# Kernel tuning notes

Measured on AMD Instinct MI355X. Metric: run time of the kernel, lower is better.

The kernel has to match this reference:

```python
import jax, jax.numpy as jnp
import numpy as np

TEMPERATURE = 0.5
EPS = 1e-12  # matches torch F.normalize default eps


def _l2_normalize(x):
    norm = jnp.sqrt(jnp.sum(x * x, axis=-1, keepdims=True))
    return x / jnp.maximum(norm, EPS)


def setup_inputs() -> dict:
    key = jax.random.key(0)
    k1, k2 = jax.random.split(key)
    B, C, D = 64, 512, 256
    visual_features = jax.random.normal(k1, (B, C, D), dtype=jnp.float32)
    text_embeddings = jax.random.normal(k2, (B, C, D), dtype=jnp.float32)
    return {"visual_features": visual_features, "text_embeddings": text_embeddings}


def reference(visual_features, text_embeddings):
    v = _l2_normalize(visual_features)   # (B, C, D)
    t = _l2_normalize(text_embeddings)   # (B, C, D)
    # positive: diagonal similarity per class
    sim_pos = jnp.einsum('bcd,bcd->bc', v, t)
    positive = jnp.exp(sim_pos / TEMPERATURE)            # (B, C)
    # full BxCxC similarity matrix
    all_sim = jnp.exp(jnp.einsum('bcd,bkd->bck', v, t) / TEMPERATURE)
    negative = jnp.sum(all_sim, axis=-1) - positive      # (B, C)
    loss = -jnp.log(positive / (positive + negative))
    return jnp.mean(loss)
```

## Files before the change

### kernel.cpp

```cpp
#include <hip/hip_runtime.h>
#include <hip/hip_bf16.h>

#define BB 64
#define CC 512
#define DD 256

typedef __attribute__((ext_vector_type(8))) short bf16x8;
typedef __attribute__((ext_vector_type(4))) float f32x4;
typedef unsigned int u32;

#define SWZ(r) (((r) & 7) << 4)

__device__ inline short f2bf(float f) {
    union { __hip_bfloat16 h; short s; } cv;
    cv.h = __float2bfloat16(f);
    return cv.s;
}

__global__ __launch_bounds__(256) void norm_rows(const float* __restrict__ in,
                                                 unsigned short* __restrict__ out) {
    const int row  = blockIdx.x * 4 + (threadIdx.x >> 6);
    const int lane = threadIdx.x & 63;
    const float4 x = reinterpret_cast<const float4*>(in)[(size_t)row * 64 + lane];
    float ss = x.x * x.x + x.y * x.y + x.z * x.z + x.w * x.w;
#pragma unroll
    for (int off = 32; off; off >>= 1) ss += __shfl_xor(ss, off);
    const float r = 1.0f / fmaxf(sqrtf(ss), 1e-12f);
    ushort4 o;
    o.x = (unsigned short)f2bf(x.x * r);
    o.y = (unsigned short)f2bf(x.y * r);
    o.z = (unsigned short)f2bf(x.z * r);
    o.w = (unsigned short)f2bf(x.w * r);
    reinterpret_cast<ushort4*>(out)[(size_t)row * 64 + lane] = o;
}

__global__ __launch_bounds__(256, 2) void gemm_loss(const float* __restrict__ V,
                                                    const unsigned short* __restrict__ Tn,
                                                    float* __restrict__ partials) {
    __shared__ char lds[65536];
    __shared__ float vred[256];
    __shared__ float dred[256];

    const int i0 = blockIdx.x;
    const int b  = (i0 & 7) * 8 + ((i0 >> 3) & 7);
    const int rb = i0 >> 6;

    const int tid  = threadIdx.x;
    const int lane = tid & 63;
    const int wave = tid >> 6;
    const int g    = lane >> 4;
    const int ln   = lane & 15;

    const float* gV = V + (size_t)b * (CC * DD) + (size_t)rb * 64 * DD;
    const char*  gT = reinterpret_cast<const char*>(Tn + (size_t)b * (CC * DD));

#pragma unroll
    for (int r2 = 0; r2 < 8; ++r2) {
        const int L  = r2 * 1024 + (lane << 4);
        const int lr = L >> 9, inrow = L & 511;
        __builtin_amdgcn_global_load_lds(
            (const u32*)(gT + (size_t)(wave * 16 + lr) * 512 + (inrow ^ SWZ(lr))),
            (u32*)(lds + wave * 8192 + r2 * 1024), 16, 0, 0);
    }

    {
        const int rrow  = tid >> 3;
        const int ecolB = (tid & 7) * 64;
        char* bufA = lds + 32768;
#pragma unroll
        for (int p = 0; p < 2; ++p) {
            const float4* src =
                reinterpret_cast<const float4*>(gV + (size_t)(p * 32 + rrow) * DD) + (tid & 7) * 8;
            float4 x[8];
#pragma unroll
            for (int q = 0; q < 8; ++q) x[q] = src[q];
            float ss = 0.f;
#pragma unroll
            for (int q = 0; q < 8; ++q)
                ss += x[q].x * x[q].x + x[q].y * x[q].y + x[q].z * x[q].z + x[q].w * x[q].w;
            ss += __shfl_xor(ss, 1);
            ss += __shfl_xor(ss, 2);
            ss += __shfl_xor(ss, 4);
            const float rinv = 1.0f / fmaxf(sqrtf(ss), 1e-12f);
            const int row = p * 32 + rrow;
            char* dstrow  = bufA + row * 512;
            const int sw  = SWZ(row);
#pragma unroll
            for (int q2 = 0; q2 < 4; ++q2) {
                const float4 v0 = x[2 * q2], v1 = x[2 * q2 + 1];
                bf16x8 o;
                o[0] = f2bf(v0.x * rinv); o[1] = f2bf(v0.y * rinv);
                o[2] = f2bf(v0.z * rinv); o[3] = f2bf(v0.w * rinv);
                o[4] = f2bf(v1.x * rinv); o[5] = f2bf(v1.y * rinv);
                o[6] = f2bf(v1.z * rinv); o[7] = f2bf(v1.w * rinv);
                *reinterpret_cast<bf16x8*>(dstrow + ((ecolB + q2 * 16) ^ sw)) = o;
            }
        }
    }
    __syncthreads();

    bf16x8 a[4][8];
#pragma unroll
    for (int i = 0; i < 4; ++i) {
        const int row  = i * 16 + ln;
        const char* rp = lds + 32768 + row * 512;
        const int sw   = SWZ(row);
#pragma unroll
        for (int kk = 0; kk < 8; ++kk)
            a[i][kk] = *reinterpret_cast<const bf16x8*>(rp + ((kk * 64 + g * 16) ^ sw));
    }
    __syncthreads();

    float rs[4][4];
    float dg[4][4];
#pragma unroll
    for (int i = 0; i < 4; ++i)
#pragma unroll
        for (int r = 0; r < 4; ++r) { rs[i][r] = 0.f; dg[i][r] = 0.f; }

    for (int ct = 0; ct < 8; ++ct) {
        if (ct < 7) {
            const char* gtile = gT + (size_t)(ct + 1) * 64 * 512;
            char* dst = lds + (((ct + 1) & 1) ? 32768 : 0) + wave * 8192;
#pragma unroll
            for (int r2 = 0; r2 < 8; ++r2) {
                const int L  = r2 * 1024 + (lane << 4);
                const int lr = L >> 9, inrow = L & 511;
                __builtin_amdgcn_global_load_lds(
                    (const u32*)(gtile + (size_t)(wave * 16 + lr) * 512 + (inrow ^ SWZ(lr))),
                    (u32*)(dst + r2 * 1024), 16, 0, 0);
            }
            asm volatile("s_waitcnt vmcnt(8)" ::: "memory");
        } else {
            asm volatile("s_waitcnt vmcnt(0)" ::: "memory");
        }

        const char* rp = lds + ((ct & 1) ? 32768 : 0) + wave * 8192 + ln * 512;
        const int sw   = SWZ(ln);
        f32x4 acc[4];
#pragma unroll
        for (int i = 0; i < 4; ++i) acc[i] = (f32x4){0.f, 0.f, 0.f, 0.f};
        __builtin_amdgcn_s_setprio(1);
#pragma unroll
        for (int kk = 0; kk < 8; ++kk) {
            const bf16x8 bb = *reinterpret_cast<const bf16x8*>(rp + ((kk * 64 + g * 16) ^ sw));
#pragma unroll
            for (int i = 0; i < 4; ++i)
                acc[i] = __builtin_amdgcn_mfma_f32_16x16x32_bf16(a[i][kk], bb, acc[i], 0, 0, 0);
        }
        __builtin_amdgcn_s_setprio(0);

        const int gcol = ct * 64 + wave * 16 + ln;
#pragma unroll
        for (int i = 0; i < 4; ++i) {
            const int grow = rb * 64 + i * 16 + g * 4;
#pragma unroll
            for (int r = 0; r < 4; ++r) {
                const float s2 = acc[i][r] * 2.0f;
                rs[i][r] += __expf(s2);
                if (ct == rb && gcol == grow + r) dg[i][r] += s2;
            }
        }
    }

#pragma unroll
    for (int i = 0; i < 4; ++i)
#pragma unroll
        for (int r = 0; r < 4; ++r) {
            float v = rs[i][r];
            float d = dg[i][r];
#pragma unroll
            for (int m = 1; m < 16; m <<= 1) {
                v += __shfl_xor(v, m);
                d += __shfl_xor(d, m);
            }
            if (ln == 0) {
                const int rl = i * 16 + g * 4 + r;
                vred[rl * 4 + wave] = v;
                dred[rl * 4 + wave] = d;
            }
        }
    __syncthreads();

    if (wave == 0) {
        const float vv =
            vred[lane * 4] + vred[lane * 4 + 1] + vred[lane * 4 + 2] + vred[lane * 4 + 3];
        const float dd =
            dred[lane * 4] + dred[lane * 4 + 1] + dred[lane * 4 + 2] + dred[lane * 4 + 3];
        float lsum = logf(vv) - dd;
#pragma unroll
        for (int m = 1; m < 64; m <<= 1) lsum += __shfl_xor(lsum, m);
        if (lane == 0) partials[i0] = lsum;
    }
}

__global__ __launch_bounds__(256) void final_reduce(const float* __restrict__ partials,
                                                    float* __restrict__ out) {
    const int t = threadIdx.x;
    float v = partials[t] + partials[t + 256];
#pragma unroll
    for (int m = 1; m < 64; m <<= 1) v += __shfl_xor(v, m);
    __shared__ float red[4];
    if ((t & 63) == 0) red[t >> 6] = v;
    __syncthreads();
    if (t == 0) out[0] = (red[0] + red[1] + red[2] + red[3]) * (1.0f / 32768.0f);
}

extern "C" void kernel_launch(void* const* d_in, const int* in_sizes, int n_in,
                              void* d_out, int out_size, void* d_ws, size_t ws_size,
                              hipStream_t stream) {
    const float* vis = (const float*)d_in[0];
    const float* txt = (const float*)d_in[1];

    unsigned short* Tn = (unsigned short*)d_ws;
    float* partials    = (float*)((char*)d_ws + (size_t)BB * CC * DD * 2);
    float* out         = (float*)d_out;

    norm_rows<<<8192, 256, 0, stream>>>(txt, Tn);
    gemm_loss<<<512, 256, 0, stream>>>(vis, Tn, partials);
    final_reduce<<<1, 256, 0, stream>>>(partials, out);
}
```

Measured before the change: 40.57 us.

## Halve LDS footprint with 2x2 wave tiling and 32-column double-buffered T tiles

Restructures gemm_loss so each block uses 32KB of LDS instead of 64KB. Waves are arranged 2x2 over the 64-row by 32-column output tile, and T is streamed in 16 tiles of 32 rows through a double buffer that reuses the A staging area. Each wave now holds half as many A fragments and accumulators, and the launch bound is raised to 4 blocks per CU to increase occupancy. The cost is more loop iterations and two explicit barriers per tile, which add synchronisation overhead.

```diff
diff --git a/kernel.cpp b/kernel.cpp
--- a/kernel.cpp
+++ b/kernel.cpp
@@ -34,12 +34,12 @@
     reinterpret_cast<ushort4*>(out)[(size_t)row * 64 + lane] = o;
 }
 
-__global__ __launch_bounds__(256, 2) void gemm_loss(const float* __restrict__ V,
+__global__ __launch_bounds__(256, 4) void gemm_loss(const float* __restrict__ V,
                                                     const unsigned short* __restrict__ Tn,
                                                     float* __restrict__ partials) {
-    __shared__ char lds[65536];
-    __shared__ float vred[256];
-    __shared__ float dred[256];
+    __shared__ char ldsb[32768];
+    __shared__ float vred[128];
+    __shared__ float dred[128];
 
     const int i0 = blockIdx.x;
     const int b  = (i0 & 7) * 8 + ((i0 >> 3) & 7);
@@ -48,25 +48,17 @@
     const int tid  = threadIdx.x;
     const int lane = tid & 63;
     const int wave = tid >> 6;
+    const int wr   = wave >> 1;
+    const int wc   = wave & 1;
     const int g    = lane >> 4;
     const int ln   = lane & 15;
 
     const float* gV = V + (size_t)b * (CC * DD) + (size_t)rb * 64 * DD;
     const char*  gT = reinterpret_cast<const char*>(Tn + (size_t)b * (CC * DD));
-
-#pragma unroll
-    for (int r2 = 0; r2 < 8; ++r2) {
-        const int L  = r2 * 1024 + (lane << 4);
-        const int lr = L >> 9, inrow = L & 511;
-        __builtin_amdgcn_global_load_lds(
-            (const u32*)(gT + (size_t)(wave * 16 + lr) * 512 + (inrow ^ SWZ(lr))),
-            (u32*)(lds + wave * 8192 + r2 * 1024), 16, 0, 0);
-    }
 
     {
         const int rrow  = tid >> 3;
         const int ecolB = (tid & 7) * 64;
-        char* bufA = lds + 32768;
 #pragma unroll
         for (int p = 0; p < 2; ++p) {
             const float4* src =
@@ -83,7 +75,7 @@
             ss += __shfl_xor(ss, 4);
             const float rinv = 1.0f / fmaxf(sqrtf(ss), 1e-12f);
             const int row = p * 32 + rrow;
-            char* dstrow  = bufA + row * 512;
+            char* dstrow  = ldsb + row * 512;
             const int sw  = SWZ(row);
 #pragma unroll
             for (int q2 = 0; q2 < 4; ++q2) {
@@ -99,11 +91,11 @@
     }
     __syncthreads();
 
-    bf16x8 a[4][8];
-#pragma unroll
-    for (int i = 0; i < 4; ++i) {
-        const int row  = i * 16 + ln;
-        const char* rp = lds + 32768 + row * 512;
+    bf16x8 a[2][8];
+#pragma unroll
+    for (int i = 0; i < 2; ++i) {
+        const int row  = wr * 32 + i * 16 + ln;
+        const char* rp = ldsb + row * 512;
         const int sw   = SWZ(row);
 #pragma unroll
         for (int kk = 0; kk < 8; ++kk)
@@ -111,60 +103,75 @@
     }
     __syncthreads();
 
-    float rs[4][4];
-    float dg[4][4];
-#pragma unroll
-    for (int i = 0; i < 4; ++i)
+#pragma unroll
+    for (int t0 = 0; t0 < 2; ++t0) {
+        const char* gtile = gT + (size_t)t0 * 32 * 512;
+        char* dst = ldsb + t0 * 16384 + wave * 4096;
+#pragma unroll
+        for (int r2 = 0; r2 < 4; ++r2) {
+            const int L  = r2 * 1024 + (lane << 4);
+            const int lr = L >> 9, inrow = L & 511;
+            __builtin_amdgcn_global_load_lds(
+                (const u32*)(gtile + (size_t)(wave * 8 + lr) * 512 + (inrow ^ SWZ(lr))),
+                (u32*)(dst + r2 * 1024), 16, 0, 0);
+        }
+    }
+
+    float rs[2][4];
+    float dg[2][4];
+#pragma unroll
+    for (int i = 0; i < 2; ++i)
 #pragma unroll
         for (int r = 0; r < 4; ++r) { rs[i][r] = 0.f; dg[i][r] = 0.f; }
 
-    for (int ct = 0; ct < 8; ++ct) {
-        if (ct < 7) {
-            const char* gtile = gT + (size_t)(ct + 1) * 64 * 512;
-            char* dst = lds + (((ct + 1) & 1) ? 32768 : 0) + wave * 8192;
-#pragma unroll
-            for (int r2 = 0; r2 < 8; ++r2) {
+    for (int t = 0; t < 16; ++t) {
+        if (t < 15) asm volatile("s_waitcnt vmcnt(4)" ::: "memory");
+        else        asm volatile("s_waitcnt vmcnt(0)" ::: "memory");
+        __builtin_amdgcn_s_barrier();
+        __builtin_amdgcn_sched_barrier(0);
+
+        const char* rp = ldsb + (t & 1) * 16384 + (wc * 16 + ln) * 512;
+        const int sw   = SWZ(ln);
+        f32x4 acc[2] = {(f32x4){0.f, 0.f, 0.f, 0.f}, (f32x4){0.f, 0.f, 0.f, 0.f}};
+        __builtin_amdgcn_s_setprio(1);
+#pragma unroll
+        for (int kk = 0; kk < 8; ++kk) {
+            const bf16x8 bb = *reinterpret_cast<const bf16x8*>(rp + ((kk * 64 + g * 16) ^ sw));
+            acc[0] = __builtin_amdgcn_mfma_f32_16x16x32_bf16(a[0][kk], bb, acc[0], 0, 0, 0);
+            acc[1] = __builtin_amdgcn_mfma_f32_16x16x32_bf16(a[1][kk], bb, acc[1], 0, 0, 0);
+        }
+        __builtin_amdgcn_s_setprio(0);
+
+        const int gcol = t * 32 + wc * 16 + ln;
+#pragma unroll
+        for (int i = 0; i < 2; ++i) {
+            const int grow = rb * 64 + wr * 32 + i * 16 + g * 4;
+#pragma unroll
+            for (int r = 0; r < 4; ++r) {
+                const float s2 = acc[i][r] * 2.0f;
+                rs[i][r] += __expf(s2);
+                if (gcol == grow + r) dg[i][r] += s2;
+            }
+        }
+
+        __builtin_amdgcn_s_barrier();
+        __builtin_amdgcn_sched_barrier(0);
+        if (t < 14) {
+            const char* gtile = gT + (size_t)(t + 2) * 32 * 512;
+            char* dst = ldsb + (t & 1) * 16384 + wave * 4096;
+#pragma unroll
+            for (int r2 = 0; r2 < 4; ++r2) {
                 const int L  = r2 * 1024 + (lane << 4);
                 const int lr = L >> 9, inrow = L & 511;
                 __builtin_amdgcn_global_load_lds(
-                    (const u32*)(gtile + (size_t)(wave * 16 + lr) * 512 + (inrow ^ SWZ(lr))),
+                    (const u32*)(gtile + (size_t)(wave * 8 + lr) * 512 + (inrow ^ SWZ(lr))),
                     (u32*)(dst + r2 * 1024), 16, 0, 0);
             }
-            asm volatile("s_waitcnt vmcnt(8)" ::: "memory");
-        } else {
-            asm volatile("s_waitcnt vmcnt(0)" ::: "memory");
-        }
-
-        const char* rp = lds + ((ct & 1) ? 32768 : 0) + wave * 8192 + ln * 512;
-        const int sw   = SWZ(ln);
-        f32x4 acc[4];
-#pragma unroll
-        for (int i = 0; i < 4; ++i) acc[i] = (f32x4){0.f, 0.f, 0.f, 0.f};
-        __builtin_amdgcn_s_setprio(1);
-#pragma unroll
-        for (int kk = 0; kk < 8; ++kk) {
-            const bf16x8 bb = *reinterpret_cast<const bf16x8*>(rp + ((kk * 64 + g * 16) ^ sw));
-#pragma unroll
-            for (int i = 0; i < 4; ++i)
-                acc[i] = __builtin_amdgcn_mfma_f32_16x16x32_bf16(a[i][kk], bb, acc[i], 0, 0, 0);
-        }
-        __builtin_amdgcn_s_setprio(0);
-
-        const int gcol = ct * 64 + wave * 16 + ln;
-#pragma unroll
-        for (int i = 0; i < 4; ++i) {
-            const int grow = rb * 64 + i * 16 + g * 4;
-#pragma unroll
-            for (int r = 0; r < 4; ++r) {
-                const float s2 = acc[i][r] * 2.0f;
-                rs[i][r] += __expf(s2);
-                if (ct == rb && gcol == grow + r) dg[i][r] += s2;
-            }
-        }
-    }
-
-#pragma unroll
-    for (int i = 0; i < 4; ++i)
+        }
+    }
+
+#pragma unroll
+    for (int i = 0; i < 2; ++i)
 #pragma unroll
         for (int r = 0; r < 4; ++r) {
             float v = rs[i][r];
@@ -175,22 +182,20 @@
                 d += __shfl_xor(d, m);
             }
             if (ln == 0) {
-                const int rl = i * 16 + g * 4 + r;
-                vred[rl * 4 + wave] = v;
-                dred[rl * 4 + wave] = d;
-            }
-        }
-    __syncthreads();
-
-    if (wave == 0) {
-        const float vv =
-            vred[lane * 4] + vred[lane * 4 + 1] + vred[lane * 4 + 2] + vred[lane * 4 + 3];
-        const float dd =
-            dred[lane * 4] + dred[lane * 4 + 1] + dred[lane * 4 + 2] + dred[lane * 4 + 3];
+                const int rl = wr * 32 + i * 16 + g * 4 + r;
+                vred[rl * 2 + wc] = v;
+                dred[rl * 2 + wc] = d;
+            }
+        }
+    __syncthreads();
+
+    if (tid < 64) {
+        const float vv = vred[tid * 2] + vred[tid * 2 + 1];
+        const float dd = dred[tid * 2] + dred[tid * 2 + 1];
         float lsum = logf(vv) - dd;
 #pragma unroll
         for (int m = 1; m < 64; m <<= 1) lsum += __shfl_xor(lsum, m);
-        if (lane == 0) partials[i0] = lsum;
+        if (tid == 0) partials[i0] = lsum;
     }
 }
 
```

Result: no change. 40.47 us (-0.2%).
